# Performance work log

Measured on AMD Instinct MI355X. Metric: run time of the kernel, lower is better.

Reference implementation:

```python
import jax, jax.numpy as jnp
import numpy as np

N_NODES = 50000
N_EDGES = 800000
IN_F = 128
OUT_F = 32
HEADS = 4
NEG_SLOPE = 0.2
EPS = 1e-8


def setup_inputs() -> dict:
    key = jax.random.key(0)
    k1, k2, k3, k4, k5 = jax.random.split(key, 5)
    x = jax.random.normal(k1, (N_NODES, IN_F), dtype=jnp.float32)
    edge_index = jax.random.randint(k2, (2, N_EDGES), 0, N_NODES, dtype=jnp.int64)
    # nn.Linear weight: (out_features*num_heads, in_features), xavier-uniform scale
    W = jax.random.normal(k3, (OUT_F * HEADS, IN_F), dtype=jnp.float32) * 0.08
    a_src = jax.random.normal(k4, (HEADS, OUT_F), dtype=jnp.float32) * 0.1
    a_dst = jax.random.normal(k5, (HEADS, OUT_F), dtype=jnp.float32) * 0.1
    return {"x": x, "edge_index": edge_index, "W": W, "a_src": a_src, "a_dst": a_dst}


def reference(x, edge_index, W, a_src, a_dst):
    # x: (N, in_f); edge_index: (2, E); W: (H*F, in_f); a_src/a_dst: (H, F)
    N = x.shape[0]
    H, F = a_src.shape
    h = (x @ W.T).reshape(N, H, F)                      # (N, H, F)
    src, dst = edge_index[0], edge_index[1]
    # per-edge attention logits (E, H)
    e_src = jnp.einsum('ehf,hf->eh', h[src], a_src)
    e_dst = jnp.einsum('ehf,hf->eh', h[dst], a_dst)
    e = jax.nn.leaky_relu(e_src + e_dst, negative_slope=NEG_SLOPE)
    # segment softmax over incoming edges of each dst node
    e_max = jax.ops.segment_max(e, dst, num_segments=N)  # (N, H); -inf for empty segments
    e_max = jnp.where(jnp.isfinite(e_max), e_max, 0.0)   # torch zeros-init; empty segments never gathered
    exp_e = jnp.exp(e - e_max[dst])
    sum_exp = jax.ops.segment_sum(exp_e, dst, num_segments=N)  # (N, H)
    attention = exp_e / (sum_exp[dst] + EPS)             # (E, H); dropout is identity at eval
    # weighted scatter-add aggregation
    messages = h[src] * attention[:, :, None]            # (E, H, F)
    out = jax.ops.segment_sum(messages, dst, num_segments=N)  # (N, H, F)
    return out.reshape(N, H * F)                         # concat=True
```

## Files before the change

### kernel.cpp

```cpp
#include <hip/hip_runtime.h>
#include <stdint.h>

#define N_NODES 50000
#define N_EDGES 800000
#define HF 128
#define NEG_SLOPE 0.2f
#define EPS_F 1e-8f
#define NBKT 196
#define NBLK 256
#define EPB (N_EDGES / NBLK)
#define BKT_N (NBKT * NBLK)
#define SCAN_A 49
#define SCAN_B 49

typedef __attribute__((ext_vector_type(8))) short short8;
typedef __attribute__((ext_vector_type(4))) float f32x4;

__device__ __forceinline__ float bf2f(unsigned short u) {
    union { unsigned int i; float f; } v; v.i = ((unsigned int)u) << 16; return v.f;
}
__device__ __forceinline__ unsigned short f2bf(float f) {
    union { unsigned int i; float f; } v; v.f = f;
    unsigned int b = v.i;
    unsigned int r = (b + 0x7FFFu + ((b >> 16) & 1u)) >> 16;
    return (unsigned short)r;
}
__device__ __forceinline__ float leaky(float v) { return v > 0.f ? v : NEG_SLOPE * v; }
__device__ __forceinline__ unsigned short f2h(float f) {
    _Float16 h = (_Float16)f; unsigned short u; __builtin_memcpy(&u, &h, 2); return u;
}
__device__ __forceinline__ float h2f(unsigned short u) {
    _Float16 h; __builtin_memcpy(&h, &u, 2); return (float)h;
}

__global__ void k_sniff(const void* x, const void* eidx, int* flags) {
    int l = threadIdx.x;
    const unsigned short* xu = (const unsigned short*)x;
    float f = bf2f(xu[2 * l]);
    float af = fabsf(f);
    bool extreme = !(af <= 1e6f) || (f != 0.0f && af < 1e-7f);
    unsigned long long mask = __ballot(extreme);
    const unsigned int* eu = (const unsigned int*)eidx;
    unsigned int w = eu[2 * l + 1];
    unsigned long long mask2 = __ballot(w != 0u);
    if (l == 0) {
        flags[0] = (__popcll(mask) >= 8) ? 0 : 1;
        flags[1] = (__popcll(mask2) >= 4) ? 0 : 1;
    }
}

__global__ __launch_bounds__(256) void k_convert(const void* W, const void* a_src, const void* a_dst,
                                                 const void* eidx, unsigned short* Wbf, float* af,
                                                 unsigned int* edgePk, int* counts, int* bh,
                                                 const int* flags) {
    __shared__ int lh[NBKT];
    int tid = threadIdx.x, blk = blockIdx.x;
    int isB = flags[0], is64 = flags[1];
    if (tid < NBKT) lh[tid] = 0;
    if (blk < 64) {
        int i = blk * 256 + tid;
        Wbf[i] = isB ? ((const unsigned short*)W)[i] : f2bf(((const float*)W)[i]);
    } else if (blk == 64 && tid < 128) {
        af[tid]       = isB ? bf2f(((const unsigned short*)a_src)[tid]) : ((const float*)a_src)[tid];
        af[128 + tid] = isB ? bf2f(((const unsigned short*)a_dst)[tid]) : ((const float*)a_dst)[tid];
    }
    __syncthreads();
    int e0 = blk * EPB;
    for (int i = tid; i < EPB; i += 256) {
        int e = e0 + i;
        int s, d;
        if (is64) {
            s = (int)((const long long*)eidx)[e];
            d = (int)((const long long*)eidx)[N_EDGES + e];
        } else {
            s = ((const int*)eidx)[e];
            d = ((const int*)eidx)[N_EDGES + e];
        }
        edgePk[e] = (unsigned int)s | ((unsigned int)d << 16);
        atomicAdd(&counts[d], 1);
        atomicAdd(&lh[d >> 8], 1);
    }
    __syncthreads();
    if (tid < NBKT) bh[tid * NBLK + blk] = lh[tid];
}

__global__ __launch_bounds__(256) void k_gemm(const void* x, const unsigned short* Wbf, const float* af,
                                              unsigned short* h, float* s_src, float* s_dst,
                                              const int* flags) {
    __shared__ short xl[64 * 136];
    __shared__ short wl[128 * 136];
    int tid = threadIdx.x;
    int isB = flags[0];
    int nb = blockIdx.x * 64;
    const unsigned short* xu = (const unsigned short*)x;
    const float* xf = (const float*)x;

    #pragma unroll
    for (int it = 0; it < 8; ++it) {
        int o = (tid >> 4) + it * 16;
        int k8 = (tid & 15) * 8;
        *(short8*)&wl[o * 136 + k8] = *(const short8*)&Wbf[o * 128 + k8];
    }
    #pragma unroll
    for (int it = 0; it < 4; ++it) {
        int row = (tid >> 4) + it * 16;
        int k8 = (tid & 15) * 8;
        int node = nb + row;
        short8 val;
        if (node < N_NODES) {
            if (isB) {
                val = *(const short8*)&xu[(size_t)node * 128 + k8];
            } else {
                float4 f0 = *(const float4*)&xf[(size_t)node * 128 + k8];
                float4 f1 = *(const float4*)&xf[(size_t)node * 128 + k8 + 4];
                val[0] = (short)f2bf(f0.x); val[1] = (short)f2bf(f0.y);
                val[2] = (short)f2bf(f0.z); val[3] = (short)f2bf(f0.w);
                val[4] = (short)f2bf(f1.x); val[5] = (short)f2bf(f1.y);
                val[6] = (short)f2bf(f1.z); val[7] = (short)f2bf(f1.w);
            }
        } else {
            val = short8{0,0,0,0,0,0,0,0};
        }
        *(short8*)&xl[row * 136 + k8] = val;
    }
    __syncthreads();

    int wv = tid >> 6, l = tid & 63;
    int lr = l & 15, lg = l >> 4;

    f32x4 acc0 = {0,0,0,0}, acc1 = {0,0,0,0}, acc2 = {0,0,0,0}, acc3 = {0,0,0,0};
    f32x4 acc4 = {0,0,0,0}, acc5 = {0,0,0,0}, acc6 = {0,0,0,0}, acc7 = {0,0,0,0};
    #pragma unroll
    for (int kb = 0; kb < 4; ++kb) {
        short8 a = *(const short8*)&xl[(wv * 16 + lr) * 136 + kb * 32 + lg * 8];
        short8 b0 = *(const short8*)&wl[(0 * 16 + lr) * 136 + kb * 32 + lg * 8];
        short8 b1 = *(const short8*)&wl[(1 * 16 + lr) * 136 + kb * 32 + lg * 8];
        short8 b2 = *(const short8*)&wl[(2 * 16 + lr) * 136 + kb * 32 + lg * 8];
        short8 b3 = *(const short8*)&wl[(3 * 16 + lr) * 136 + kb * 32 + lg * 8];
        short8 b4 = *(const short8*)&wl[(4 * 16 + lr) * 136 + kb * 32 + lg * 8];
        short8 b5 = *(const short8*)&wl[(5 * 16 + lr) * 136 + kb * 32 + lg * 8];
        short8 b6 = *(const short8*)&wl[(6 * 16 + lr) * 136 + kb * 32 + lg * 8];
        short8 b7 = *(const short8*)&wl[(7 * 16 + lr) * 136 + kb * 32 + lg * 8];
        acc0 = __builtin_amdgcn_mfma_f32_16x16x32_bf16(a, b0, acc0, 0, 0, 0);
        acc1 = __builtin_amdgcn_mfma_f32_16x16x32_bf16(a, b1, acc1, 0, 0, 0);
        acc2 = __builtin_amdgcn_mfma_f32_16x16x32_bf16(a, b2, acc2, 0, 0, 0);
        acc3 = __builtin_amdgcn_mfma_f32_16x16x32_bf16(a, b3, acc3, 0, 0, 0);
        acc4 = __builtin_amdgcn_mfma_f32_16x16x32_bf16(a, b4, acc4, 0, 0, 0);
        acc5 = __builtin_amdgcn_mfma_f32_16x16x32_bf16(a, b5, acc5, 0, 0, 0);
        acc6 = __builtin_amdgcn_mfma_f32_16x16x32_bf16(a, b6, acc6, 0, 0, 0);
        acc7 = __builtin_amdgcn_mfma_f32_16x16x32_bf16(a, b7, acc7, 0, 0, 0);
    }

    float pS[4][4], pD[4][4];
    #pragma unroll
    for (int r = 0; r < 4; ++r)
        #pragma unroll
        for (int hd = 0; hd < 4; ++hd) { pS[r][hd] = 0.f; pD[r][hd] = 0.f; }

    #define EPI(OT, ACC) { \
        float aSv = af[(OT) * 16 + lr]; \
        float aDv = af[128 + (OT) * 16 + lr]; \
        _Pragma("unroll") \
        for (int r = 0; r < 4; ++r) { \
            int n = nb + wv * 16 + lg * 4 + r; \
            float v = ACC[r]; \
            if (n < N_NODES) h[(size_t)n * HF + (OT) * 16 + lr] = f2bf(v); \
            pS[r][(OT) >> 1] += v * aSv; \
            pD[r][(OT) >> 1] += v * aDv; \
        } }
    EPI(0, acc0) EPI(1, acc1) EPI(2, acc2) EPI(3, acc3)
    EPI(4, acc4) EPI(5, acc5) EPI(6, acc6) EPI(7, acc7)
    #undef EPI

    #pragma unroll
    for (int off = 1; off < 16; off <<= 1) {
        #pragma unroll
        for (int r = 0; r < 4; ++r)
            #pragma unroll
            for (int hd = 0; hd < 4; ++hd) {
                pS[r][hd] += __shfl_xor(pS[r][hd], off, 64);
                pD[r][hd] += __shfl_xor(pD[r][hd], off, 64);
            }
    }
    if (lr == 0) {
        #pragma unroll
        for (int r = 0; r < 4; ++r) {
            int n = nb + wv * 16 + lg * 4 + r;
            if (n < N_NODES) {
                #pragma unroll
                for (int hd = 0; hd < 4; ++hd) {
                    s_src[n * 4 + hd] = pS[r][hd];
                    s_dst[n * 4 + hd] = pD[r][hd];
                }
            }
        }
    }
}

__global__ __launch_bounds__(1024) void k_scanA(const int* cA, int* oA, int* bA,
                                                const int* cB, int* oB, int* bB) {
    __shared__ int buf[1024];
    int t = threadIdx.x;
    bool second = blockIdx.x >= SCAN_A;
    int blk = second ? (int)blockIdx.x - SCAN_A : (int)blockIdx.x;
    const int* c = second ? cB : cA;
    int* o = second ? oB : oA;
    int* bt = second ? bB : bA;
    int n = second ? BKT_N : N_NODES;
    int i = blk * 1024 + t;
    int v = (i < n) ? c[i] : 0;
    buf[t] = v;
    __syncthreads();
    for (int off = 1; off < 1024; off <<= 1) {
        int u = (t >= off) ? buf[t - off] : 0;
        __syncthreads();
        buf[t] += u;
        __syncthreads();
    }
    if (i < n) o[i] = buf[t] - v;
    if (t == 1023) bt[blk] = buf[1023];
}

__global__ void k_scanB(int* btA, int* oA, int* btB, int* oB) {
    int w = threadIdx.x >> 6, l = threadIdx.x & 63;
    int* bt = w ? btB : btA;
    int* o  = w ? oB : oA;
    int nblk = w ? SCAN_B : SCAN_A;
    int n    = w ? BKT_N : N_NODES;
    int v = (l < nblk) ? bt[l] : 0;
    int inc = v;
    for (int off = 1; off < 64; off <<= 1) {
        int u = __shfl_up(inc, off, 64);
        if (l >= off) inc += u;
    }
    int tot = __shfl(inc, nblk - 1, 64);
    if (l < nblk) bt[l] = inc - v;
    if (l == 0) o[n] = tot;
}

__global__ __launch_bounds__(256) void k_bucket1(const unsigned int* edgePk, const int* base,
                                                 const int* btot2, unsigned int* bkt) {
    __shared__ int lcur[NBKT];
    int tid = threadIdx.x, blk = blockIdx.x;
    if (tid < NBKT) {
        int idx = tid * NBLK + blk;
        lcur[tid] = base[idx] + btot2[idx >> 10];
    }
    __syncthreads();
    int e0 = blk * EPB;
    for (int i = tid; i < EPB; i += 256) {
        unsigned int pk = edgePk[e0 + i];
        int slot = atomicAdd(&lcur[pk >> 24], 1);
        bkt[slot] = pk;
    }
}

__global__ __launch_bounds__(256) void k_bucket2(const unsigned int* bkt, const int* base,
                                                 const int* btot2, const int* rowSt, const int* btot,
                                                 const float* s_src, const float* s_dst, uint4* recs) {
    __shared__ int lcur[256];
    int tid = threadIdx.x, bk = blockIdx.x;
    lcur[tid] = 0;
    __syncthreads();
    int i0 = bk * NBLK;
    int bstart = base[i0] + btot2[i0 >> 10];
    int i1 = (bk + 1) * NBLK;
    int bend = (i1 < BKT_N) ? (base[i1] + btot2[i1 >> 10]) : base[BKT_N];
    for (int i = bstart + tid; i < bend; i += 256) {
        unsigned int pk = bkt[i];
        int s = (int)(pk & 0xFFFFu), d = (int)(pk >> 16);
        int r = atomicAdd(&lcur[d & 255], 1);
        int slot = rowSt[d] + btot[d >> 10] + r;
        float4 ss = *(const float4*)&s_src[s * 4];
        float4 sd = *(const float4*)&s_dst[d * 4];
        unsigned int q0 = f2h(leaky(ss.x + sd.x));
        unsigned int q1 = f2h(leaky(ss.y + sd.y));
        unsigned int q2 = f2h(leaky(ss.z + sd.z));
        unsigned int q3 = f2h(leaky(ss.w + sd.w));
        uint4 rc;
        rc.x = (unsigned int)s;
        rc.y = q0 | (q1 << 16);
        rc.z = q2 | (q3 << 16);
        rc.w = 0u;
        recs[slot] = rc;
    }
}

__global__ __launch_bounds__(256) void k_agg(const unsigned short* h, const uint4* recs,
                                             const int* rowSt, const int* btot, float* out) {
    int wid = threadIdx.x >> 6;
    int l = threadIdx.x & 63;
    int n = blockIdx.x * 4 + wid;
    if (n >= N_NODES) return;
    int rs = rowSt[n] + btot[n >> 10];
    int re = (n + 1 < N_NODES) ? (rowSt[n + 1] + btot[(n + 1) >> 10]) : rowSt[N_NODES];
    int deg = re - rs;
    int lf = l & 15, grp = l >> 4, hd = lf >> 2;
    if (deg == 0) {
        *(float2*)&out[(size_t)n * HF + lf * 8 + grp * 2] = make_float2(0.f, 0.f);
        return;
    }
    const float NI = -__builtin_inff();
    float z = 0.f;
    float a0=0,a1=0,a2=0,a3=0,a4=0,a5=0,a6=0,a7=0;

    float sc = NI; int si = 0;
    if (grp < deg) {
        uint4 r = recs[rs + grp];
        si = (int)r.x;
        sc = h2f((unsigned short)((((hd & 2) ? r.z : r.y)) >> ((hd & 1) * 16)));
    }
    uint4 u = *(const uint4*)&h[(size_t)si * HF + lf * 8];

    for (int it = 0; it < deg; it += 4) {
        int e1 = it + 4 + grp;
        float sc1 = NI; int si1 = 0;
        if (e1 < deg) {
            uint4 r = recs[rs + e1];
            si1 = (int)r.x;
            sc1 = h2f((unsigned short)((((hd & 2) ? r.z : r.y)) >> ((hd & 1) * 16)));
        }
        uint4 u1 = *(const uint4*)&h[(size_t)si1 * HF + lf * 8];
        float w = __expf(fminf(sc, 60.f));
        z += w;
        a0 += w * bf2f((unsigned short)(u.x & 0xFFFFu)); a1 += w * bf2f((unsigned short)(u.x >> 16));
        a2 += w * bf2f((unsigned short)(u.y & 0xFFFFu)); a3 += w * bf2f((unsigned short)(u.y >> 16));
        a4 += w * bf2f((unsigned short)(u.z & 0xFFFFu)); a5 += w * bf2f((unsigned short)(u.z >> 16));
        a6 += w * bf2f((unsigned short)(u.w & 0xFFFFu)); a7 += w * bf2f((unsigned short)(u.w >> 16));
        sc = sc1; si = si1; u = u1;
    }
    #pragma unroll
    for (int off = 16; off <= 32; off <<= 1) {
        z  += __shfl_xor(z,  off, 64);
        a0 += __shfl_xor(a0, off, 64); a1 += __shfl_xor(a1, off, 64);
        a2 += __shfl_xor(a2, off, 64); a3 += __shfl_xor(a3, off, 64);
        a4 += __shfl_xor(a4, off, 64); a5 += __shfl_xor(a5, off, 64);
        a6 += __shfl_xor(a6, off, 64); a7 += __shfl_xor(a7, off, 64);
    }
    float inv = 1.0f / (z + EPS_F);
    if (grp == 0) *(float4*)&out[(size_t)n * HF + lf * 8]     = make_float4(a0*inv, a1*inv, a2*inv, a3*inv);
    if (grp == 1) *(float4*)&out[(size_t)n * HF + lf * 8 + 4] = make_float4(a4*inv, a5*inv, a6*inv, a7*inv);
}

extern "C" void kernel_launch(void* const* d_in, const int* in_sizes, int n_in,
                              void* d_out, int out_size, void* d_ws, size_t ws_size,
                              hipStream_t stream) {
    const void* x     = d_in[0];
    const void* eidx  = d_in[1];
    const void* W     = d_in[2];
    const void* a_src = d_in[3];
    const void* a_dst = d_in[4];
    char* ws = (char*)d_ws;

    size_t off = 0;
    auto alloc = [&](size_t bytes) { size_t o = off; off += (bytes + 255) & ~(size_t)255; return o; };
    size_t flagsO  = alloc(64 * 4);
    size_t countsO = alloc((size_t)N_NODES * 4);
    size_t zeroEnd = off;
    size_t rowO    = alloc((size_t)(N_NODES + 1) * 4);
    size_t btotO   = alloc(64 * 4);
    size_t btot2O  = alloc(64 * 4);
    size_t bhO     = alloc((size_t)BKT_N * 4);
    size_t baseO   = alloc((size_t)(BKT_N + 1) * 4);
    size_t epkO    = alloc((size_t)N_EDGES * 4);
    size_t bktO    = alloc((size_t)N_EDGES * 4);
    size_t recsO   = alloc((size_t)N_EDGES * 16);
    size_t WbO     = alloc(16384 * 2);
    size_t afO     = alloc(256 * 4);
    size_t ssO     = alloc((size_t)N_NODES * 4 * 4);
    size_t sdO     = alloc((size_t)N_NODES * 4 * 4);
    size_t hO      = alloc((size_t)N_NODES * HF * 2);
    (void)ws_size; (void)in_sizes; (void)n_in;

    int*   flags   = (int*)(ws + flagsO);
    int*   counts  = (int*)(ws + countsO);
    int*   rowSt   = (int*)(ws + rowO);
    int*   btot    = (int*)(ws + btotO);
    int*   btot2   = (int*)(ws + btot2O);
    int*   bh      = (int*)(ws + bhO);
    int*   base    = (int*)(ws + baseO);
    unsigned int* edgePk = (unsigned int*)(ws + epkO);
    unsigned int* bkt    = (unsigned int*)(ws + bktO);
    uint4* recs    = (uint4*)(ws + recsO);
    unsigned short* Wbf = (unsigned short*)(ws + WbO);
    float* af      = (float*)(ws + afO);
    float* s_src   = (float*)(ws + ssO);
    float* s_dst   = (float*)(ws + sdO);
    unsigned short* h = (unsigned short*)(ws + hO);
    float* outF    = (float*)d_out;

    hipMemsetAsync(ws + countsO, 0, zeroEnd - countsO, stream);

    k_sniff<<<1, 64, 0, stream>>>(x, eidx, flags);
    k_convert<<<NBLK, 256, 0, stream>>>(W, a_src, a_dst, eidx, Wbf, af, edgePk, counts, bh, flags);
    k_gemm<<<(N_NODES + 63) / 64, 256, 0, stream>>>(x, Wbf, af, h, s_src, s_dst, flags);
    k_scanA<<<SCAN_A + SCAN_B, 1024, 0, stream>>>(counts, rowSt, btot, bh, base, btot2);
    k_scanB<<<1, 128, 0, stream>>>(btot, rowSt, btot2, base);
    k_bucket1<<<NBLK, 256, 0, stream>>>(edgePk, base, btot2, bkt);
    k_bucket2<<<NBKT, 256, 0, stream>>>(bkt, base, btot2, rowSt, btot, s_src, s_dst, recs);
    k_agg<<<(N_NODES + 3) / 4, 256, 0, stream>>>(h, recs, rowSt, btot, outF);
}
```

Baseline: 195.2 us.

## Derive CSR row starts inside bucket pass and fold sniff into consumers

```diff
diff --git a/kernel.cpp b/kernel.cpp
--- a/kernel.cpp
+++ b/kernel.cpp
@@ -10,7 +10,6 @@
 #define NBLK 256
 #define EPB (N_EDGES / NBLK)
 #define BKT_N (NBKT * NBLK)
-#define SCAN_A 49
 #define SCAN_B 49
 
 typedef __attribute__((ext_vector_type(8))) short short8;
@@ -32,31 +31,34 @@
 __device__ __forceinline__ float h2f(unsigned short u) {
     _Float16 h; __builtin_memcpy(&h, &u, 2); return (float)h;
 }
-
-__global__ void k_sniff(const void* x, const void* eidx, int* flags) {
-    int l = threadIdx.x;
-    const unsigned short* xu = (const unsigned short*)x;
-    float f = bf2f(xu[2 * l]);
-    float af = fabsf(f);
-    bool extreme = !(af <= 1e6f) || (f != 0.0f && af < 1e-7f);
-    unsigned long long mask = __ballot(extreme);
-    const unsigned int* eu = (const unsigned int*)eidx;
-    unsigned int w = eu[2 * l + 1];
-    unsigned long long mask2 = __ballot(w != 0u);
-    if (l == 0) {
-        flags[0] = (__popcll(mask) >= 8) ? 0 : 1;
-        flags[1] = (__popcll(mask2) >= 4) ? 0 : 1;
+__device__ __forceinline__ void sniff_wave(const void* x, const void* eidx, int tid,
+                                           volatile int* sf) {
+    if (tid < 64) {
+        const unsigned short* xu = (const unsigned short*)x;
+        float f = bf2f(xu[2 * tid]);
+        float af = fabsf(f);
+        bool extreme = !(af <= 1e6f) || (f != 0.0f && af < 1e-7f);
+        unsigned long long mask = __ballot(extreme);
+        if (eidx) {
+            const unsigned int* eu = (const unsigned int*)eidx;
+            unsigned long long mask2 = __ballot(eu[2 * tid + 1] != 0u);
+            if (tid == 0) sf[1] = (__popcll(mask2) >= 4) ? 0 : 1;
+        }
+        if (tid == 0) sf[0] = (__popcll(mask) >= 8) ? 0 : 1;
     }
 }
 
 __global__ __launch_bounds__(256) void k_convert(const void* W, const void* a_src, const void* a_dst,
-                                                 const void* eidx, unsigned short* Wbf, float* af,
-                                                 unsigned int* edgePk, int* counts, int* bh,
-                                                 const int* flags) {
+                                                 const void* x, const void* eidx,
+                                                 unsigned short* Wbf, float* af,
+                                                 unsigned int* edgePk, int* bh) {
     __shared__ int lh[NBKT];
+    __shared__ int sf[2];
     int tid = threadIdx.x, blk = blockIdx.x;
-    int isB = flags[0], is64 = flags[1];
     if (tid < NBKT) lh[tid] = 0;
+    sniff_wave(x, eidx, tid, sf);
+    __syncthreads();
+    int isB = sf[0], is64 = sf[1];
     if (blk < 64) {
         int i = blk * 256 + tid;
         Wbf[i] = isB ? ((const unsigned short*)W)[i] : f2bf(((const float*)W)[i]);
@@ -64,7 +66,6 @@
         af[tid]       = isB ? bf2f(((const unsigned short*)a_src)[tid]) : ((const float*)a_src)[tid];
         af[128 + tid] = isB ? bf2f(((const unsigned short*)a_dst)[tid]) : ((const float*)a_dst)[tid];
     }
-    __syncthreads();
     int e0 = blk * EPB;
     for (int i = tid; i < EPB; i += 256) {
         int e = e0 + i;
@@ -77,7 +78,6 @@
             d = ((const int*)eidx)[N_EDGES + e];
         }
         edgePk[e] = (unsigned int)s | ((unsigned int)d << 16);
-        atomicAdd(&counts[d], 1);
         atomicAdd(&lh[d >> 8], 1);
     }
     __syncthreads();
@@ -85,15 +85,18 @@
 }
 
 __global__ __launch_bounds__(256) void k_gemm(const void* x, const unsigned short* Wbf, const float* af,
-                                              unsigned short* h, float* s_src, float* s_dst,
-                                              const int* flags) {
+                                              unsigned short* h, float* s_src, float* s_dst) {
     __shared__ short xl[64 * 136];
     __shared__ short wl[128 * 136];
+    __shared__ int sf[2];
     int tid = threadIdx.x;
-    int isB = flags[0];
     int nb = blockIdx.x * 64;
     const unsigned short* xu = (const unsigned short*)x;
     const float* xf = (const float*)x;
+
+    sniff_wave(x, nullptr, tid, sf);
+    __syncthreads();
+    int isB = sf[0];
 
     #pragma unroll
     for (int it = 0; it < 8; ++it) {
@@ -197,18 +200,11 @@
     }
 }
 
-__global__ __launch_bounds__(1024) void k_scanA(const int* cA, int* oA, int* bA,
-                                                const int* cB, int* oB, int* bB) {
+__global__ __launch_bounds__(1024) void k_scanA(const int* c, int* o, int* bt) {
     __shared__ int buf[1024];
     int t = threadIdx.x;
-    bool second = blockIdx.x >= SCAN_A;
-    int blk = second ? (int)blockIdx.x - SCAN_A : (int)blockIdx.x;
-    const int* c = second ? cB : cA;
-    int* o = second ? oB : oA;
-    int* bt = second ? bB : bA;
-    int n = second ? BKT_N : N_NODES;
-    int i = blk * 1024 + t;
-    int v = (i < n) ? c[i] : 0;
+    int i = blockIdx.x * 1024 + t;
+    int v = (i < BKT_N) ? c[i] : 0;
     buf[t] = v;
     __syncthreads();
     for (int off = 1; off < 1024; off <<= 1) {
@@ -217,25 +213,19 @@
         buf[t] += u;
         __syncthreads();
     }
-    if (i < n) o[i] = buf[t] - v;
-    if (t == 1023) bt[blk] = buf[1023];
-}
-
-__global__ void k_scanB(int* btA, int* oA, int* btB, int* oB) {
-    int w = threadIdx.x >> 6, l = threadIdx.x & 63;
-    int* bt = w ? btB : btA;
-    int* o  = w ? oB : oA;
-    int nblk = w ? SCAN_B : SCAN_A;
-    int n    = w ? BKT_N : N_NODES;
-    int v = (l < nblk) ? bt[l] : 0;
+    if (i < BKT_N) o[i] = buf[t] - v;
+    if (t == 1023) bt[blockIdx.x] = buf[1023];
+}
+
+__global__ void k_scanB(int* bt) {
+    int l = threadIdx.x;
+    int v = (l < SCAN_B) ? bt[l] : 0;
     int inc = v;
     for (int off = 1; off < 64; off <<= 1) {
         int u = __shfl_up(inc, off, 64);
         if (l >= off) inc += u;
     }
-    int tot = __shfl(inc, nblk - 1, 64);
-    if (l < nblk) bt[l] = inc - v;
-    if (l == 0) o[n] = tot;
+    if (l < SCAN_B) bt[l] = inc - v;
 }
 
 __global__ __launch_bounds__(256) void k_bucket1(const unsigned int* edgePk, const int* base,
@@ -256,21 +246,41 @@
 }
 
 __global__ __launch_bounds__(256) void k_bucket2(const unsigned int* bkt, const int* base,
-                                                 const int* btot2, const int* rowSt, const int* btot,
+                                                 const int* btot2, int* rowSt,
                                                  const float* s_src, const float* s_dst, uint4* recs) {
+    __shared__ int lhist[256];
+    __shared__ int buf[256];
+    __shared__ int lexcl[256];
     __shared__ int lcur[256];
     int tid = threadIdx.x, bk = blockIdx.x;
-    lcur[tid] = 0;
+    lhist[tid] = 0; lcur[tid] = 0;
     __syncthreads();
     int i0 = bk * NBLK;
     int bstart = base[i0] + btot2[i0 >> 10];
     int i1 = (bk + 1) * NBLK;
-    int bend = (i1 < BKT_N) ? (base[i1] + btot2[i1 >> 10]) : base[BKT_N];
+    int bend = (i1 < BKT_N) ? (base[i1] + btot2[i1 >> 10]) : N_EDGES;
+    for (int i = bstart + tid; i < bend; i += 256)
+        atomicAdd(&lhist[(bkt[i] >> 16) & 255], 1);
+    __syncthreads();
+    int v = lhist[tid];
+    buf[tid] = v;
+    __syncthreads();
+    for (int off = 1; off < 256; off <<= 1) {
+        int u = (tid >= off) ? buf[tid - off] : 0;
+        __syncthreads();
+        buf[tid] += u;
+        __syncthreads();
+    }
+    lexcl[tid] = buf[tid] - v;
+    int node = bk * 256 + tid;
+    if (node < N_NODES) rowSt[node] = bstart + lexcl[tid];
+    __syncthreads();
     for (int i = bstart + tid; i < bend; i += 256) {
         unsigned int pk = bkt[i];
-        int s = (int)(pk & 0xFFFFu), d = (int)(pk >> 16);
-        int r = atomicAdd(&lcur[d & 255], 1);
-        int slot = rowSt[d] + btot[d >> 10] + r;
+        int s = (int)(pk & 0xFFFFu), d8 = (int)((pk >> 16) & 255);
+        int r = atomicAdd(&lcur[d8], 1);
+        int slot = bstart + lexcl[d8] + r;
+        int d = (int)(pk >> 16);
         float4 ss = *(const float4*)&s_src[s * 4];
         float4 sd = *(const float4*)&s_dst[d * 4];
         unsigned int q0 = f2h(leaky(ss.x + sd.x));
@@ -287,13 +297,13 @@
 }
 
 __global__ __launch_bounds__(256) void k_agg(const unsigned short* h, const uint4* recs,
-                                             const int* rowSt, const int* btot, float* out) {
+                                             const int* rowSt, float* out) {
     int wid = threadIdx.x >> 6;
     int l = threadIdx.x & 63;
     int n = blockIdx.x * 4 + wid;
     if (n >= N_NODES) return;
-    int rs = rowSt[n] + btot[n >> 10];
-    int re = (n + 1 < N_NODES) ? (rowSt[n + 1] + btot[(n + 1) >> 10]) : rowSt[N_NODES];
+    int rs = rowSt[n];
+    int re = (n + 1 < N_NODES) ? rowSt[n + 1] : N_EDGES;
     int deg = re - rs;
     int lf = l & 15, grp = l >> 4, hd = lf >> 2;
     if (deg == 0) {
@@ -354,11 +364,7 @@
 
     size_t off = 0;
     auto alloc = [&](size_t bytes) { size_t o = off; off += (bytes + 255) & ~(size_t)255; return o; };
-    size_t flagsO  = alloc(64 * 4);
-    size_t countsO = alloc((size_t)N_NODES * 4);
-    size_t zeroEnd = off;
     size_t rowO    = alloc((size_t)(N_NODES + 1) * 4);
-    size_t btotO   = alloc(64 * 4);
     size_t btot2O  = alloc(64 * 4);
     size_t bhO     = alloc((size_t)BKT_N * 4);
     size_t baseO   = alloc((size_t)(BKT_N + 1) * 4);
@@ -372,10 +378,7 @@
     size_t hO      = alloc((size_t)N_NODES * HF * 2);
     (void)ws_size; (void)in_sizes; (void)n_in;
 
-    int*   flags   = (int*)(ws + flagsO);
-    int*   counts  = (int*)(ws + countsO);
     int*   rowSt   = (int*)(ws + rowO);
-    int*   btot    = (int*)(ws + btotO);
     int*   btot2   = (int*)(ws + btot2O);
     int*   bh      = (int*)(ws + bhO);
     int*   base    = (int*)(ws + baseO);
@@ -389,14 +392,11 @@
     unsigned short* h = (unsigned short*)(ws + hO);
     float* outF    = (float*)d_out;
 
-    hipMemsetAsync(ws + countsO, 0, zeroEnd - countsO, stream);
-
-    k_sniff<<<1, 64, 0, stream>>>(x, eidx, flags);
-    k_convert<<<NBLK, 256, 0, stream>>>(W, a_src, a_dst, eidx, Wbf, af, edgePk, counts, bh, flags);
-    k_gemm<<<(N_NODES + 63) / 64, 256, 0, stream>>>(x, Wbf, af, h, s_src, s_dst, flags);
-    k_scanA<<<SCAN_A + SCAN_B, 1024, 0, stream>>>(counts, rowSt, btot, bh, base, btot2);
-    k_scanB<<<1, 128, 0, stream>>>(btot, rowSt, btot2, base);
+    k_convert<<<NBLK, 256, 0, stream>>>(W, a_src, a_dst, x, eidx, Wbf, af, edgePk, bh);
+    k_gemm<<<(N_NODES + 63) / 64, 256, 0, stream>>>(x, Wbf, af, h, s_src, s_dst);
+    k_scanA<<<SCAN_B, 1024, 0, stream>>>(bh, base, btot2);
+    k_scanB<<<1, 64, 0, stream>>>(btot2);
     k_bucket1<<<NBLK, 256, 0, stream>>>(edgePk, base, btot2, bkt);
-    k_bucket2<<<NBKT, 256, 0, stream>>>(bkt, base, btot2, rowSt, btot, s_src, s_dst, recs);
-    k_agg<<<(N_NODES + 3) / 4, 256, 0, stream>>>(h, recs, rowSt, btot, outF);
-}
+    k_bucket2<<<NBKT, 256, 0, stream>>>(bkt, base, btot2, rowSt, s_src, s_dst, recs);
+    k_agg<<<(N_NODES + 3) / 4, 256, 0, stream>>>(h, recs, rowSt, outF);
+}
```

Result: faster. 166.2 us (-14.8%).
